# Performance work log

Measured on AMD Instinct MI355X. Metric: run time of the kernel, lower is better.

The kernel has to match this reference:

```python
import jax, jax.numpy as jnp
import numpy as np

TEMP = 0.5
EPS = 1e-12  # matches torch F.normalize default eps


def _l2_normalize(x):
    n = jnp.sqrt(jnp.sum(x * x, axis=1, keepdims=True))
    return x / jnp.maximum(n, EPS)


def setup_inputs() -> dict:
    key = jax.random.key(0)
    k1, k2 = jax.random.split(key)
    B, D = 4096, 256
    return {
        "x_i": jax.random.normal(k1, (B, D), dtype=jnp.float32),
        "x_j": jax.random.normal(k2, (B, D), dtype=jnp.float32),
    }


def reference(x_i, x_j):
    B = x_i.shape[0]
    z = jnp.concatenate([_l2_normalize(x_i), _l2_normalize(x_j)], axis=0)  # [2B, D]
    # cosine similarity of normalized vectors == plain matmul
    sim = z @ z.T  # [2B, 2B]
    pos = jnp.concatenate([jnp.diagonal(sim, B), jnp.diagonal(sim, -B)], axis=0)  # [2B]
    neg_mask = 1.0 - jnp.eye(2 * B, dtype=sim.dtype)
    denom = jnp.sum(neg_mask * jnp.exp(sim / TEMP), axis=1)  # [2B]
    # -log(exp(pos/T) / denom) = -pos/T + log(denom)
    loss = jnp.sum(-(pos / TEMP) + jnp.log(denom)) / (2 * B)
    return loss
```

## Files before the change

kernel.cpp:

```cpp
#include <hip/hip_runtime.h>
#include <hip/hip_bf16.h>

#define B_ROWS 4096
#define NROWS  8192
#define D      256
#define TT     264
#define NBLK2  512

typedef __attribute__((ext_vector_type(8))) short bf16x8;
typedef __attribute__((ext_vector_type(4))) float floatx4;

__global__ __launch_bounds__(256) void norm_pos_kernel(
    const float* __restrict__ xi, const float* __restrict__ xj,
    short* __restrict__ z, float* __restrict__ pos,
    float* __restrict__ selfdot, float* __restrict__ rowsum,
    float* __restrict__ out, unsigned int* __restrict__ counter) {
    int gt = blockIdx.x * 256 + threadIdx.x;
    if (gt < NROWS) rowsum[gt] = 0.f;
    if (gt == 0) { out[0] = 0.f; counter[0] = 0u; }

    int p    = blockIdx.x * 4 + (threadIdx.x >> 6);
    int lane = threadIdx.x & 63;
    float4 v1 = ((const float4*)(xi + (size_t)p * D))[lane];
    float4 v2 = ((const float4*)(xj + (size_t)p * D))[lane];
    float ss1 = v1.x * v1.x + v1.y * v1.y + v1.z * v1.z + v1.w * v1.w;
    float ss2 = v2.x * v2.x + v2.y * v2.y + v2.z * v2.z + v2.w * v2.w;
#pragma unroll
    for (int off = 32; off > 0; off >>= 1) {
        ss1 += __shfl_xor(ss1, off);
        ss2 += __shfl_xor(ss2, off);
    }
    float sc1 = 1.0f / fmaxf(sqrtf(ss1), 1e-12f);
    float sc2 = 1.0f / fmaxf(sqrtf(ss2), 1e-12f);

    union { __hip_bfloat16 h[4]; short4 s4; } u1, u2;
    u1.h[0] = __float2bfloat16(v1.x * sc1); u1.h[1] = __float2bfloat16(v1.y * sc1);
    u1.h[2] = __float2bfloat16(v1.z * sc1); u1.h[3] = __float2bfloat16(v1.w * sc1);
    u2.h[0] = __float2bfloat16(v2.x * sc2); u2.h[1] = __float2bfloat16(v2.y * sc2);
    u2.h[2] = __float2bfloat16(v2.z * sc2); u2.h[3] = __float2bfloat16(v2.w * sc2);
    ((short4*)(z + (size_t)p * D))[lane]            = u1.s4;
    ((short4*)(z + (size_t)(p + B_ROWS) * D))[lane] = u2.s4;

    float sd1 = 0.f, sd2 = 0.f, dp = 0.f;
#pragma unroll
    for (int j = 0; j < 4; j++) {
        float a = __bfloat162float(u1.h[j]);
        float b = __bfloat162float(u2.h[j]);
        sd1 += a * a; sd2 += b * b; dp += a * b;
    }
#pragma unroll
    for (int off = 32; off > 0; off >>= 1) {
        sd1 += __shfl_xor(sd1, off);
        sd2 += __shfl_xor(sd2, off);
        dp  += __shfl_xor(dp,  off);
    }
    if (lane == 0) {
        pos[p] = dp; pos[p + B_ROWS] = dp;
        selfdot[p] = sd1; selfdot[p + B_ROWS] = sd2;
    }
}

__global__ __launch_bounds__(256, 2) void sim_rowsum_kernel(
    const short* __restrict__ z, float* __restrict__ rowsum,
    const float* __restrict__ pos, const float* __restrict__ selfdot,
    unsigned int* __restrict__ counter, float* __restrict__ out) {
    __shared__ unsigned int done_s;
    __shared__ float sdata[4];

    const int tid  = threadIdx.x;
    const int lane = tid & 63;
    const int w    = tid >> 6;
    const int lm   = lane & 15;
    const int lg   = lane >> 4;

    const int s   = blockIdx.x >> 5;
    const int q   = blockIdx.x & 31;
    const int L0  = 256 - 8 * s;
    const int cb  = (q * TT) >> 5;
    const int ce  = ((q + 1) * TT) >> 5;

    bf16x8 a[8][4];
    floatx4 acc[4][2];
    float rsacc[4][4];

#pragma unroll
    for (int mi = 0; mi < 4; mi++)
#pragma unroll
        for (int r = 0; r < 4; r++) rsacc[mi][r] = 0.f;

    auto decode = [&](int c, int& panel, int& colbase, bool& mirror) {
        int cloc;
        if (c < L0) { panel = s;      cloc = c; }
        else        { panel = 31 - s; cloc = c - L0; }
        colbase = panel * 256 + cloc * 32;
        mirror  = (cloc >= 8);
    };

    auto loadA = [&](int panel) {
#pragma unroll
        for (int kk = 0; kk < 8; kk++)
#pragma unroll
            for (int mi = 0; mi < 4; mi++)
                a[kk][mi] = *(const bf16x8*)(
                    z + (size_t)(panel * 256 + w * 64 + mi * 16 + lm) * D +
                    kk * 32 + lg * 8);
    };

    auto flushRs = [&](int panel) {
#pragma unroll
        for (int mi = 0; mi < 4; mi++)
#pragma unroll
            for (int r = 0; r < 4; r++) {
                float v = rsacc[mi][r];
                v += __shfl_xor(v, 1); v += __shfl_xor(v, 2);
                v += __shfl_xor(v, 4); v += __shfl_xor(v, 8);
                if (lm == 0)
                    atomicAdd(&rowsum[panel * 256 + w * 64 + mi * 16 + lg * 4 + r], v);
                rsacc[mi][r] = 0.f;
            }
    };

    int panel, colbase; bool mirror;
    decode(cb, panel, colbase, mirror);
    int curpanel = panel;
    loadA(panel);

    for (int c = cb; c < ce; c++) {
        decode(c, panel, colbase, mirror);

        if (panel != curpanel) {
            flushRs(curpanel);
            loadA(panel);
            curpanel = panel;
        }

#pragma unroll
        for (int mi = 0; mi < 4; mi++)
#pragma unroll
            for (int ni = 0; ni < 2; ni++)
                acc[mi][ni] = (floatx4){0.f, 0.f, 0.f, 0.f};

        const short* bbase = z + (size_t)colbase * D;
#pragma unroll
        for (int kk = 0; kk < 8; kk++) {
            bf16x8 b0 = *(const bf16x8*)(
                bbase + (size_t)lm * D + kk * 32 + lg * 8);
            bf16x8 b1 = *(const bf16x8*)(
                bbase + (size_t)(16 + lm) * D + kk * 32 + lg * 8);
#pragma unroll
            for (int mi = 0; mi < 4; mi++)
                acc[mi][0] = __builtin_amdgcn_mfma_f32_16x16x32_bf16(
                    a[kk][mi], b0, acc[mi][0], 0, 0, 0);
#pragma unroll
            for (int mi = 0; mi < 4; mi++)
                acc[mi][1] = __builtin_amdgcn_mfma_f32_16x16x32_bf16(
                    a[kk][mi], b1, acc[mi][1], 0, 0, 0);
        }

        float cs0 = 0.f, cs1 = 0.f;
#pragma unroll
        for (int mi = 0; mi < 4; mi++)
#pragma unroll
            for (int r = 0; r < 4; r++) {
                float e0 = __expf(2.0f * acc[mi][0][r]);
                float e1 = __expf(2.0f * acc[mi][1][r]);
                rsacc[mi][r] += e0 + e1;
                cs0 += e0; cs1 += e1;
            }
        if (mirror) {
            cs0 += __shfl_xor(cs0, 16); cs0 += __shfl_xor(cs0, 32);
            cs1 += __shfl_xor(cs1, 16); cs1 += __shfl_xor(cs1, 32);
            if (lane < 16) {
                atomicAdd(&rowsum[colbase + lane],      cs0);
                atomicAdd(&rowsum[colbase + 16 + lane], cs1);
            }
        }
    }
    flushRs(curpanel);

    __syncthreads();
    if (tid == 0) {
        __threadfence();
        done_s = atomicAdd(counter, 1u);
    }
    __syncthreads();
    if (done_s == (unsigned int)(NBLK2 - 1)) {
        __threadfence();
        float acc_l = 0.f;
#pragma unroll 4
        for (int r = tid; r < NROWS; r += 256) {
            float rsv = __hip_atomic_load(&rowsum[r], __ATOMIC_RELAXED,
                                          __HIP_MEMORY_SCOPE_AGENT);
            float denom = rsv - __expf(2.0f * selfdot[r]);
            acc_l += -2.0f * pos[r] + logf(denom);
        }
#pragma unroll
        for (int off = 32; off > 0; off >>= 1) acc_l += __shfl_xor(acc_l, off);
        if (lane == 0) sdata[w] = acc_l;
        __syncthreads();
        if (tid == 0)
            out[0] = (sdata[0] + sdata[1] + sdata[2] + sdata[3]) / (float)NROWS;
    }
}

extern "C" void kernel_launch(void* const* d_in, const int* in_sizes, int n_in,
                              void* d_out, int out_size, void* d_ws, size_t ws_size,
                              hipStream_t stream) {
    const float* xi = (const float*)d_in[0];
    const float* xj = (const float*)d_in[1];
    float* out      = (float*)d_out;

    char* ws        = (char*)d_ws;
    short* z        = (short*)ws;
    float* rowsum   = (float*)(ws + (size_t)NROWS * D * 2);
    float* pos      = rowsum + NROWS;
    float* selfdot  = pos + NROWS;
    unsigned int* counter = (unsigned int*)(selfdot + NROWS);

    norm_pos_kernel<<<B_ROWS / 4, 256, 0, stream>>>(xi, xj, z, pos, selfdot,
                                                    rowsum, out, counter);
    sim_rowsum_kernel<<<NBLK2, 256, 0, stream>>>(z, rowsum, pos, selfdot,
                                                 counter, out);
}
```

Measured before the change: 118.9 us.

## Stage B column tiles into swizzled LDS via async global_load_lds prefetch

Each wave now copies the next 32-column B tile into its own swizzled LDS buffer using direct global-to-LDS loads, issued after the current tile's MFMAs. The intent is to overlap the B fetch with the exp/rowsum epilogue and to replace strided global reads with conflict-free LDS reads. It uses a single buffer per wave and hand-placed waitcnt instructions, so it adds 64KB of LDS per block, which may reduce occupancy. It also risks ordering hazards if the vmcnt accounting, which counts the mirror-path atomics, is wrong.

```diff
diff --git a/kernel.cpp b/kernel.cpp
--- a/kernel.cpp
+++ b/kernel.cpp
@@ -64,6 +64,7 @@
     const short* __restrict__ z, float* __restrict__ rowsum,
     const float* __restrict__ pos, const float* __restrict__ selfdot,
     unsigned int* __restrict__ counter, float* __restrict__ out) {
+    __shared__ __align__(16) short Bbuf[4][8192];
     __shared__ unsigned int done_s;
     __shared__ float sdata[4];
 
@@ -72,6 +73,7 @@
     const int w    = tid >> 6;
     const int lm   = lane & 15;
     const int lg   = lane >> 4;
+    const int fxor = lm & 7;
 
     const int s   = blockIdx.x >> 5;
     const int q   = blockIdx.x & 31;
@@ -94,6 +96,13 @@
         else        { panel = 31 - s; cloc = c - L0; }
         colbase = panel * 256 + cloc * 32;
         mirror  = (cloc >= 8);
+    };
+
+    auto decodeCol = [&](int c) {
+        int cloc, panel;
+        if (c < L0) { panel = s;      cloc = c; }
+        else        { panel = 31 - s; cloc = c - L0; }
+        return panel * 256 + cloc * 32;
     };
 
     auto loadA = [&](int panel) {
@@ -120,13 +129,32 @@
             }
     };
 
+    auto stage = [&](int colbase) {
+#pragma unroll
+        for (int j = 0; j < 16; j++) {
+            int col = j * 2 + (lane >> 5);
+            int c16 = (lane & 31) ^ (col & 7);
+            const short* src = z + (size_t)(colbase + col) * D + c16 * 8;
+            __builtin_amdgcn_global_load_lds(
+                (const __attribute__((address_space(1))) unsigned int*)src,
+                (__attribute__((address_space(3))) unsigned int*)
+                    &Bbuf[w][j * 512],
+                16, 0, 0);
+        }
+    };
+
     int panel, colbase; bool mirror;
     decode(cb, panel, colbase, mirror);
     int curpanel = panel;
+    stage(colbase);
     loadA(panel);
+    bool pm = false;
 
     for (int c = cb; c < ce; c++) {
         decode(c, panel, colbase, mirror);
+
+        if (pm) asm volatile("s_waitcnt vmcnt(2)" ::: "memory");
+        else    asm volatile("s_waitcnt vmcnt(0)" ::: "memory");
 
         if (panel != curpanel) {
             flushRs(curpanel);
@@ -140,13 +168,12 @@
             for (int ni = 0; ni < 2; ni++)
                 acc[mi][ni] = (floatx4){0.f, 0.f, 0.f, 0.f};
 
-        const short* bbase = z + (size_t)colbase * D;
 #pragma unroll
         for (int kk = 0; kk < 8; kk++) {
             bf16x8 b0 = *(const bf16x8*)(
-                bbase + (size_t)lm * D + kk * 32 + lg * 8);
+                &Bbuf[w][(((lm) * 32) + ((kk * 4 + lg) ^ fxor)) * 8]);
             bf16x8 b1 = *(const bf16x8*)(
-                bbase + (size_t)(16 + lm) * D + kk * 32 + lg * 8);
+                &Bbuf[w][(((16 + lm) * 32) + ((kk * 4 + lg) ^ fxor)) * 8]);
 #pragma unroll
             for (int mi = 0; mi < 4; mi++)
                 acc[mi][0] = __builtin_amdgcn_mfma_f32_16x16x32_bf16(
@@ -156,6 +183,10 @@
                 acc[mi][1] = __builtin_amdgcn_mfma_f32_16x16x32_bf16(
                     a[kk][mi], b1, acc[mi][1], 0, 0, 0);
         }
+
+        asm volatile("s_waitcnt lgkmcnt(0)" ::: "memory");
+        if (c + 1 < ce)
+            stage(decodeCol(c + 1));
 
         float cs0 = 0.f, cs1 = 0.f;
 #pragma unroll
@@ -175,6 +206,7 @@
                 atomicAdd(&rowsum[colbase + 16 + lane], cs1);
             }
         }
+        pm = mirror;
     }
     flushRs(curpanel);
 
```

New measurement: 103.8 us. 1.15x faster.
